# Kernel optimization log

Hardware: AMD Instinct MI355X
Metric: run time of the kernel (lower is better)

Reference implementation:

```python
import jax, jax.numpy as jnp
import numpy as np

B = 256
D_MODEL = 2048
EXPAND = 4
D_INNER = EXPAND * D_MODEL  # 8192
D_STATE = 16
D_CONV = 4
DT_RANK = (D_MODEL + 15) // 16  # 128


def setup_inputs() -> dict:
    key = jax.random.key(0)
    ks = jax.random.split(key, 12)
    s = 0.02  # weight scale
    return {
        "x": jax.random.normal(ks[0], (B, 1, D_MODEL), jnp.float32),
        "conv_state": jax.random.normal(ks[1], (B, D_INNER, D_CONV), jnp.float32),
        "ssm_state": jax.random.normal(ks[2], (B, D_INNER, D_STATE), jnp.float32),
        "W_in": jax.random.normal(ks[3], (2 * D_INNER, D_MODEL), jnp.float32) * s,
        "conv_w": jax.random.normal(ks[4], (D_INNER, D_CONV), jnp.float32) * s,
        "conv_b": jax.random.normal(ks[5], (D_INNER,), jnp.float32) * s,
        "W_xproj": jax.random.normal(ks[6], (DT_RANK + 2 * D_STATE, D_INNER), jnp.float32) * s,
        "W_dt": jax.random.normal(ks[7], (D_INNER, DT_RANK), jnp.float32) * s,
        "b_dt": jax.random.normal(ks[8], (D_INNER,), jnp.float32) * s,
        "A_log": jnp.log(jax.random.uniform(ks[9], (D_INNER, D_STATE), jnp.float32, 0.5, 8.0)),
        "D_param": jax.random.normal(ks[10], (D_INNER,), jnp.float32),
        "W_out": jax.random.normal(ks[11], (D_MODEL, D_INNER), jnp.float32) * s,
    }


def reference(x, conv_state, ssm_state, W_in, conv_w, conv_b, W_xproj,
              W_dt, b_dt, A_log, D_param, W_out):
    # x: (B, 1, d_model) -> single-token Mamba.step
    xz = x[:, 0, :] @ W_in.T                      # (B, 2*d_inner)
    xi, z = jnp.split(xz, 2, axis=-1)             # (B, d_inner) each

    # depthwise conv state update (roll left, append new token)
    conv_state = jnp.concatenate([conv_state[:, :, 1:], xi[:, :, None]], axis=-1)
    xc = jnp.sum(conv_state * conv_w[None, :, :], axis=-1) + conv_b  # (B, d_inner)
    xc = jax.nn.silu(xc)

    # input-dependent SSM params
    x_db = xc @ W_xproj.T                          # (B, dt_rank + 2*d_state)
    dt = x_db[:, :DT_RANK]
    Bm = x_db[:, DT_RANK:DT_RANK + D_STATE]        # (B, d_state)
    Cm = x_db[:, DT_RANK + D_STATE:]               # (B, d_state)
    dt = jax.nn.softplus(dt @ W_dt.T + b_dt)       # (B, d_inner)

    # discretize + single-step state update
    A = -jnp.exp(A_log)                            # (d_inner, d_state)
    dA = jnp.exp(dt[:, :, None] * A[None])         # (B, d_inner, d_state)
    dB = dt[:, :, None] * Bm[:, None, :]           # (B, d_inner, d_state)
    ssm_state = ssm_state * dA + xc[:, :, None] * dB

    y = jnp.einsum('bdn,bn->bd', ssm_state, Cm) + D_param * xc
    y = y * jax.nn.silu(z)
    out = (y @ W_out.T)[:, None, :]                # (B, 1, d_model)
    return out, conv_state, ssm_state
```

## Files before the change

kernel.cpp:

```cpp
#include <hip/hip_runtime.h>
#include <hip/hip_bf16.h>

typedef __attribute__((ext_vector_type(8))) short   sv8;
typedef __attribute__((ext_vector_type(8))) __bf16  bfv8;
typedef __attribute__((ext_vector_type(4))) float   f32x4;

__device__ __forceinline__ short f2bf(float f) {
  union { float f; unsigned u; } v; v.f = f;
  unsigned r = v.u + 0x7fffu + ((v.u >> 16) & 1u);
  return (short)(r >> 16);
}

__device__ __forceinline__ f32x4 mfma16x16x32(sv8 a, sv8 b, f32x4 c) {
  return __builtin_amdgcn_mfma_f32_16x16x32_bf16(
      __builtin_bit_cast(bfv8, a), __builtin_bit_cast(bfv8, b), c, 0, 0, 0);
}

__device__ __forceinline__ float silu(float x) { return x / (1.f + __expf(-x)); }

template<int EPI>
__global__ __launch_bounds__(256) void gemm_bt(
    const float* __restrict__ A, const float* __restrict__ B, float* __restrict__ C,
    const float* __restrict__ bias, int lda, int ldb, int ldc, int kIters,
    int kStride, long cSlice)
{
  __shared__ short As[128 * 72];
  __shared__ short Bs[64 * 72];
  const int tid = threadIdx.x;
  A += (long)blockIdx.z * kStride;
  B += (long)blockIdx.z * kStride;
  C += (long)blockIdx.z * cSlice;
  const int rowA0 = blockIdx.y * 128, colB0 = blockIdx.x * 64;
  const int c4 = tid & 15, r0 = tid >> 4;
  const int wave = tid >> 6, lane = tid & 63;
  const int wm = (wave >> 1) * 64, wn = (wave & 1) * 32;
  const int lrow = lane & 15, lq = lane >> 4;
  f32x4 acc[4][2] = {};
  float4 pa[8], pb[4];

  const float* Aptr = &A[(long)(rowA0 + r0) * lda + c4 * 4];
  const float* Bptr = &B[(long)(colB0 + r0) * ldb + c4 * 4];

#pragma unroll
  for (int i = 0; i < 8; ++i) pa[i] = *(const float4*)&Aptr[(long)(16 * i) * lda];
#pragma unroll
  for (int i = 0; i < 4; ++i) pb[i] = *(const float4*)&Bptr[(long)(16 * i) * ldb];

  for (int kb = 0; kb < kIters; ++kb) {
#pragma unroll
    for (int i = 0; i < 8; ++i) {
      short4 s; s.x = f2bf(pa[i].x); s.y = f2bf(pa[i].y); s.z = f2bf(pa[i].z); s.w = f2bf(pa[i].w);
      *(short4*)&As[(r0 + 16 * i) * 72 + c4 * 4] = s;
    }
#pragma unroll
    for (int i = 0; i < 4; ++i) {
      short4 s; s.x = f2bf(pb[i].x); s.y = f2bf(pb[i].y); s.z = f2bf(pb[i].z); s.w = f2bf(pb[i].w);
      *(short4*)&Bs[(r0 + 16 * i) * 72 + c4 * 4] = s;
    }
    __syncthreads();
    if (kb + 1 < kIters) {
      const long ko = (long)(kb + 1) * 64;
#pragma unroll
      for (int i = 0; i < 8; ++i) pa[i] = *(const float4*)&Aptr[(long)(16 * i) * lda + ko];
#pragma unroll
      for (int i = 0; i < 4; ++i) pb[i] = *(const float4*)&Bptr[(long)(16 * i) * ldb + ko];
    }
#pragma unroll
    for (int ks = 0; ks < 2; ++ks) {
      const int kk = ks * 32 + lq * 8;
      sv8 af[4], bfr[2];
#pragma unroll
      for (int s = 0; s < 4; ++s) af[s] = *(const sv8*)&As[(wm + s * 16 + lrow) * 72 + kk];
#pragma unroll
      for (int s = 0; s < 2; ++s) bfr[s] = *(const sv8*)&Bs[(wn + s * 16 + lrow) * 72 + kk];
#pragma unroll
      for (int sm = 0; sm < 4; ++sm)
#pragma unroll
        for (int sn = 0; sn < 2; ++sn)
          acc[sm][sn] = mfma16x16x32(af[sm], bfr[sn], acc[sm][sn]);
    }
    __syncthreads();
  }
#pragma unroll
  for (int sm = 0; sm < 4; ++sm) {
    const int row = rowA0 + wm + sm * 16 + lq * 4;
#pragma unroll
    for (int sn = 0; sn < 2; ++sn) {
      const int col = colB0 + wn + sn * 16 + lrow;
#pragma unroll
      for (int r = 0; r < 4; ++r) {
        float v = acc[sm][sn][r];
        if (EPI == 1) { v += bias[col]; v = (v > 20.f) ? v : log1pf(__expf(v)); }
        C[(long)(row + r) * ldc + col] = v;
      }
    }
  }
}

__global__ __launch_bounds__(256) void conv_step(
    const float* __restrict__ xz, const float* __restrict__ cs_in,
    const float* __restrict__ conv_w, const float* __restrict__ conv_b,
    float* __restrict__ cs_out, float* __restrict__ xc)
{
  const long i = (long)blockIdx.x * 256 + threadIdx.x;
  const int b = (int)(i >> 13), d = (int)(i & 8191);
  const float4 c = *(const float4*)&cs_in[i * 4];
  const float4 w = *(const float4*)&conv_w[(long)d * 4];
  const float xi = xz[(long)b * 16384 + d];
  float4 nc; nc.x = c.y; nc.y = c.z; nc.z = c.w; nc.w = xi;
  *(float4*)&cs_out[i * 4] = nc;
  const float v = nc.x * w.x + nc.y * w.y + nc.z * w.z + nc.w * w.w + conv_b[d];
  xc[i] = silu(v);
}

__global__ void zero_kernel(float* p) { p[blockIdx.x * 256 + threadIdx.x] = 0.f; }

__global__ __launch_bounds__(256) void gemm_xdb(
    const float* __restrict__ xc, const float* __restrict__ W, float* __restrict__ out)
{
  __shared__ short As[256 * 72];
  __shared__ short Bs[16 * 72];
  const int tid = threadIdx.x;
  const int nt = blockIdx.x;
  const long kbase = (long)blockIdx.y * 512;
  const int c4 = tid & 15, r0 = tid >> 4;
  const int wave = tid >> 6, lane = tid & 63;
  const int lrow = lane & 15, lq = lane >> 4;
  f32x4 acc[4] = {};
  for (int kb = 0; kb < 8; ++kb) {
    const long k0 = kbase + kb * 64;
#pragma unroll
    for (int i = 0; i < 16; ++i) {
      const int r = r0 + 16 * i;
      const float4 v = *(const float4*)&xc[(long)r * 8192 + k0 + c4 * 4];
      short4 s; s.x = f2bf(v.x); s.y = f2bf(v.y); s.z = f2bf(v.z); s.w = f2bf(v.w);
      *(short4*)&As[r * 72 + c4 * 4] = s;
    }
    {
      const float4 v = *(const float4*)&W[(long)(nt * 16 + r0) * 8192 + k0 + c4 * 4];
      short4 s; s.x = f2bf(v.x); s.y = f2bf(v.y); s.z = f2bf(v.z); s.w = f2bf(v.w);
      *(short4*)&Bs[r0 * 72 + c4 * 4] = s;
    }
    __syncthreads();
#pragma unroll
    for (int ks = 0; ks < 2; ++ks) {
      const int kk = ks * 32 + lq * 8;
      const sv8 bfr = *(const sv8*)&Bs[lrow * 72 + kk];
#pragma unroll
      for (int s = 0; s < 4; ++s) {
        const sv8 af = *(const sv8*)&As[((wave * 4 + s) * 16 + lrow) * 72 + kk];
        acc[s] = mfma16x16x32(af, bfr, acc[s]);
      }
    }
    __syncthreads();
  }
  const int n = nt * 16 + lrow;
#pragma unroll
  for (int s = 0; s < 4; ++s) {
    const int m0 = (wave * 4 + s) * 16 + lq * 4;
#pragma unroll
    for (int r = 0; r < 4; ++r) atomicAdd(&out[(long)(m0 + r) * 160 + n], acc[s][r]);
  }
}

__global__ __launch_bounds__(256) void ssm_step(
    const float* __restrict__ ssm_in, const float* __restrict__ x_db,
    const float* __restrict__ dtv, const float* __restrict__ xcw,
    const float* __restrict__ xz, const float* __restrict__ A_log,
    const float* __restrict__ D_param, float* __restrict__ ssm_out, float* __restrict__ y)
{
  const long t = (long)blockIdx.x * 256 + threadIdx.x;
  const long bd = t >> 2; const int sq = (int)(t & 3);
  const int b = (int)(bd >> 13), d = (int)(bd & 8191);
  const float dt = dtv[bd];
  const float xc = xcw[bd];
  const float4 al = *(const float4*)&A_log[(long)d * 16 + sq * 4];
  const float4 st = *(const float4*)&ssm_in[bd * 16 + sq * 4];
  const float4 Bv = *(const float4*)&x_db[(long)b * 160 + 128 + sq * 4];
  const float4 Cv = *(const float4*)&x_db[(long)b * 160 + 144 + sq * 4];
  const float xdt = xc * dt;
  float4 ns;
  ns.x = st.x * __expf(dt * -__expf(al.x)) + xdt * Bv.x;
  ns.y = st.y * __expf(dt * -__expf(al.y)) + xdt * Bv.y;
  ns.z = st.z * __expf(dt * -__expf(al.z)) + xdt * Bv.z;
  ns.w = st.w * __expf(dt * -__expf(al.w)) + xdt * Bv.w;
  *(float4*)&ssm_out[bd * 16 + sq * 4] = ns;
  float part = ns.x * Cv.x + ns.y * Cv.y + ns.z * Cv.z + ns.w * Cv.w;
  part += __shfl_xor(part, 1);
  part += __shfl_xor(part, 2);
  if (sq == 0) {
    const float z = xz[(long)b * 16384 + 8192 + d];
    float yv = part + D_param[d] * xc;
    y[bd] = yv * silu(z);
  }
}

__global__ __launch_bounds__(256) void reduce8(const float* __restrict__ p, float* __restrict__ out)
{
  const long i = (long)blockIdx.x * 256 + threadIdx.x;
  float4 s = {0.f, 0.f, 0.f, 0.f};
#pragma unroll
  for (int j = 0; j < 8; ++j) {
    const float4 v = *(const float4*)&p[(long)j * 524288 + i * 4];
    s.x += v.x; s.y += v.y; s.z += v.z; s.w += v.w;
  }
  *(float4*)&out[i * 4] = s;
}

extern "C" void kernel_launch(void* const* d_in, const int* in_sizes, int n_in,
                              void* d_out, int out_size, void* d_ws, size_t ws_size,
                              hipStream_t stream) {
  const float* x        = (const float*)d_in[0];
  const float* conv_in  = (const float*)d_in[1];
  const float* ssm_in   = (const float*)d_in[2];
  const float* W_in     = (const float*)d_in[3];
  const float* conv_w   = (const float*)d_in[4];
  const float* conv_b   = (const float*)d_in[5];
  const float* W_xproj  = (const float*)d_in[6];
  const float* W_dt     = (const float*)d_in[7];
  const float* b_dt     = (const float*)d_in[8];
  const float* A_log    = (const float*)d_in[9];
  const float* D_param  = (const float*)d_in[10];
  const float* W_out    = (const float*)d_in[11];

  float* out      = (float*)d_out;
  float* conv_out = out + 524288;
  float* ssm_out  = out + 8912896;

  float* ws   = (float*)d_ws;
  float* xz   = ws;
  float* xcw  = ws + 4194304;
  float* x_db = ws + 6291456;
  float* dtv  = ws + 6332416;
  float* yv   = ws + 8429568;
  float* partials = xz;

  gemm_bt<0><<<dim3(256, 2, 1), 256, 0, stream>>>(x, W_in, xz, nullptr, 2048, 2048, 16384, 32, 0, 0);
  conv_step<<<8192, 256, 0, stream>>>(xz, conv_in, conv_w, conv_b, conv_out, xcw);
  zero_kernel<<<160, 256, 0, stream>>>(x_db);
  gemm_xdb<<<dim3(10, 16), 256, 0, stream>>>(xcw, W_xproj, x_db);
  gemm_bt<1><<<dim3(128, 2, 1), 256, 0, stream>>>(x_db, W_dt, dtv, b_dt, 160, 128, 8192, 2, 0, 0);
  ssm_step<<<32768, 256, 0, stream>>>(ssm_in, x_db, dtv, xcw, xz, A_log, D_param, ssm_out, yv);
  gemm_bt<0><<<dim3(32, 2, 8), 256, 0, stream>>>(yv, W_out, partials, nullptr, 8192, 8192, 2048, 16, 1024, 524288);
  reduce8<<<512, 256, 0, stream>>>(partials, out);
}
```

Measured before the change: 550.5 us.

## Use 512-thread GEMM blocks with double-buffered register prefetch

The shared GEMM kernel now runs 8 waves per 128x64 tile instead of 4, so each wave owns a 32x32 sub-tile and fewer accumulators. Global loads use two alternating register sets, with the next K slice prefetched while the current one is consumed, to hide latency and raise occupancy. The price is extra __syncthreads per K step, since there is still only one shared buffer. The loop steps by 2 and relies on kIters being even, which holds for all current call sites.

```diff
diff --git a/kernel.cpp b/kernel.cpp
--- a/kernel.cpp
+++ b/kernel.cpp
@@ -19,7 +19,7 @@
 __device__ __forceinline__ float silu(float x) { return x / (1.f + __expf(-x)); }
 
 template<int EPI>
-__global__ __launch_bounds__(256) void gemm_bt(
+__global__ __launch_bounds__(512, 4) void gemm_bt(
     const float* __restrict__ A, const float* __restrict__ B, float* __restrict__ C,
     const float* __restrict__ bias, int lda, int ldb, int ldc, int kIters,
     int kStride, long cSlice)
@@ -33,56 +33,68 @@
   const int rowA0 = blockIdx.y * 128, colB0 = blockIdx.x * 64;
   const int c4 = tid & 15, r0 = tid >> 4;
   const int wave = tid >> 6, lane = tid & 63;
-  const int wm = (wave >> 1) * 64, wn = (wave & 1) * 32;
+  const int wm = (wave >> 1) * 32, wn = (wave & 1) * 32;
   const int lrow = lane & 15, lq = lane >> 4;
-  f32x4 acc[4][2] = {};
-  float4 pa[8], pb[4];
+  f32x4 acc[2][2] = {};
+  float4 a0[4], b0[2], a1[4], b1[2];
 
   const float* Aptr = &A[(long)(rowA0 + r0) * lda + c4 * 4];
   const float* Bptr = &B[(long)(colB0 + r0) * ldb + c4 * 4];
 
-#pragma unroll
-  for (int i = 0; i < 8; ++i) pa[i] = *(const float4*)&Aptr[(long)(16 * i) * lda];
-#pragma unroll
-  for (int i = 0; i < 4; ++i) pb[i] = *(const float4*)&Bptr[(long)(16 * i) * ldb];
-
-  for (int kb = 0; kb < kIters; ++kb) {
-#pragma unroll
-    for (int i = 0; i < 8; ++i) {
+  auto loadS = [&](float4* pa, float4* pb, long ko) {
+#pragma unroll
+    for (int i = 0; i < 4; ++i) pa[i] = *(const float4*)&Aptr[(long)(32 * i) * lda + ko];
+#pragma unroll
+    for (int i = 0; i < 2; ++i) pb[i] = *(const float4*)&Bptr[(long)(32 * i) * ldb + ko];
+  };
+  auto stageS = [&](const float4* pa, const float4* pb) {
+#pragma unroll
+    for (int i = 0; i < 4; ++i) {
       short4 s; s.x = f2bf(pa[i].x); s.y = f2bf(pa[i].y); s.z = f2bf(pa[i].z); s.w = f2bf(pa[i].w);
-      *(short4*)&As[(r0 + 16 * i) * 72 + c4 * 4] = s;
-    }
-#pragma unroll
-    for (int i = 0; i < 4; ++i) {
+      *(short4*)&As[(r0 + 32 * i) * 72 + c4 * 4] = s;
+    }
+#pragma unroll
+    for (int i = 0; i < 2; ++i) {
       short4 s; s.x = f2bf(pb[i].x); s.y = f2bf(pb[i].y); s.z = f2bf(pb[i].z); s.w = f2bf(pb[i].w);
-      *(short4*)&Bs[(r0 + 16 * i) * 72 + c4 * 4] = s;
-    }
-    __syncthreads();
-    if (kb + 1 < kIters) {
-      const long ko = (long)(kb + 1) * 64;
-#pragma unroll
-      for (int i = 0; i < 8; ++i) pa[i] = *(const float4*)&Aptr[(long)(16 * i) * lda + ko];
-#pragma unroll
-      for (int i = 0; i < 4; ++i) pb[i] = *(const float4*)&Bptr[(long)(16 * i) * ldb + ko];
-    }
+      *(short4*)&Bs[(r0 + 32 * i) * 72 + c4 * 4] = s;
+    }
+  };
+  auto mfmaPhase = [&]() {
 #pragma unroll
     for (int ks = 0; ks < 2; ++ks) {
       const int kk = ks * 32 + lq * 8;
-      sv8 af[4], bfr[2];
-#pragma unroll
-      for (int s = 0; s < 4; ++s) af[s] = *(const sv8*)&As[(wm + s * 16 + lrow) * 72 + kk];
+      sv8 af[2], bfr[2];
+#pragma unroll
+      for (int s = 0; s < 2; ++s) af[s]  = *(const sv8*)&As[(wm + s * 16 + lrow) * 72 + kk];
 #pragma unroll
       for (int s = 0; s < 2; ++s) bfr[s] = *(const sv8*)&Bs[(wn + s * 16 + lrow) * 72 + kk];
 #pragma unroll
-      for (int sm = 0; sm < 4; ++sm)
+      for (int sm = 0; sm < 2; ++sm)
 #pragma unroll
         for (int sn = 0; sn < 2; ++sn)
           acc[sm][sn] = mfma16x16x32(af[sm], bfr[sn], acc[sm][sn]);
     }
-    __syncthreads();
-  }
-#pragma unroll
-  for (int sm = 0; sm < 4; ++sm) {
+  };
+
+  loadS(a0, b0, 0);
+  if (kIters > 1) loadS(a1, b1, 64);
+  stageS(a0, b0);
+
+  for (int kb = 0; kb < kIters; kb += 2) {
+    __syncthreads();
+    if (kb + 2 < kIters) loadS(a0, b0, (long)(kb + 2) * 64);
+    mfmaPhase();
+    __syncthreads();
+    stageS(a1, b1);
+    __syncthreads();
+    if (kb + 3 < kIters) loadS(a1, b1, (long)(kb + 3) * 64);
+    mfmaPhase();
+    __syncthreads();
+    if (kb + 2 < kIters) stageS(a0, b0);
+  }
+
+#pragma unroll
+  for (int sm = 0; sm < 2; ++sm) {
     const int row = rowA0 + wm + sm * 16 + lq * 4;
 #pragma unroll
     for (int sn = 0; sn < 2; ++sn) {
@@ -235,12 +247,12 @@
   float* yv   = ws + 8429568;
   float* partials = xz;
 
-  gemm_bt<0><<<dim3(256, 2, 1), 256, 0, stream>>>(x, W_in, xz, nullptr, 2048, 2048, 16384, 32, 0, 0);
+  gemm_bt<0><<<dim3(256, 2, 1), 512, 0, stream>>>(x, W_in, xz, nullptr, 2048, 2048, 16384, 32, 0, 0);
   conv_step<<<8192, 256, 0, stream>>>(xz, conv_in, conv_w, conv_b, conv_out, xcw);
   zero_kernel<<<160, 256, 0, stream>>>(x_db);
   gemm_xdb<<<dim3(10, 16), 256, 0, stream>>>(xcw, W_xproj, x_db);
-  gemm_bt<1><<<dim3(128, 2, 1), 256, 0, stream>>>(x_db, W_dt, dtv, b_dt, 160, 128, 8192, 2, 0, 0);
+  gemm_bt<1><<<dim3(128, 2, 1), 512, 0, stream>>>(x_db, W_dt, dtv, b_dt, 160, 128, 8192, 2, 0, 0);
   ssm_step<<<32768, 256, 0, stream>>>(ssm_in, x_db, dtv, xcw, xz, A_log, D_param, ssm_out, yv);
-  gemm_bt<0><<<dim3(32, 2, 8), 256, 0, stream>>>(yv, W_out, partials, nullptr, 8192, 8192, 2048, 16, 1024, 524288);
+  gemm_bt<0><<<dim3(32, 2, 8), 512, 0, stream>>>(yv, W_out, partials, nullptr, 8192, 8192, 2048, 16, 1024, 524288);
   reduce8<<<512, 256, 0, stream>>>(partials, out);
 }
```

Result: no change. 550.6 us (+0.0%).
